# Optimization experiments

Measured on AMD Instinct MI355X. Metric: run time of the kernel, lower is better.

## Reference

```python
import jax, jax.numpy as jnp
import numpy as np

BATCH, D, N = 16, 128, 16
E = N * (N - 1) // 2  # 120 candidate edges (strict upper triangle)


def _incidence(A, n):
    """Build edge-incidence matrices G, H of shape [b, n, E] from binary edge
    vector A [b, E] over the strict upper triangle of an n x n adjacency."""
    r, c = np.triu_indices(n, k=1)
    mask = (A > 0).astype(jnp.float32)  # [b, E]
    node = jnp.arange(n)[:, None]       # [n, 1]
    G = (node == jnp.asarray(r)[None, :]).astype(jnp.float32)[None] * mask[:, None, :]
    H = (node == jnp.asarray(c)[None, :]).astype(jnp.float32)[None] * mask[:, None, :]
    return G, H


def _kron(t1, t2):
    """Batched Kronecker product: t1 [b,r1,c1], t2 [b,r2,c2] -> [b,r1*r2,c1*c2]."""
    b, r1, c1 = t1.shape
    _, r2, c2 = t2.shape
    return (t1[:, :, None, :, None] * t2[:, None, :, None, :]).reshape(b, r1 * r2, c1 * c2)


def setup_inputs() -> dict:
    key = jax.random.key(0)
    ks = jax.random.split(key, 8)
    A_src = jax.random.randint(ks[0], (BATCH, E), 0, 2, dtype=jnp.int32)
    A_tgt = jax.random.randint(ks[1], (BATCH, E), 0, 2, dtype=jnp.int32)
    F_src = jax.random.normal(ks[2], (BATCH, D, N), dtype=jnp.float32)
    F_tgt = jax.random.normal(ks[3], (BATCH, D, N), dtype=jnp.float32)
    U_src = jax.random.normal(ks[4], (BATCH, N, N), dtype=jnp.float32)
    U_tgt = jax.random.normal(ks[5], (BATCH, N, N), dtype=jnp.float32)
    stdv = 1.0 / np.sqrt(D * 2)
    eye_half = jnp.eye(D, dtype=jnp.float32) / 2.0
    lambda1 = jax.random.uniform(ks[6], (D, D), jnp.float32, -stdv, stdv) + eye_half
    lambda2 = jax.random.uniform(ks[7], (D, D), jnp.float32, -stdv, stdv) + eye_half
    return {"A_src": A_src, "A_tgt": A_tgt, "F_src": F_src, "F_tgt": F_tgt,
            "U_src": U_src, "U_tgt": U_tgt, "lambda1": lambda1, "lambda2": lambda2}


def reference(A_src, A_tgt, F_src, F_tgt, U_src, U_tgt, lambda1, lambda2):
    b = F_src.shape[0]
    n, m = F_src.shape[-1], F_tgt.shape[-1]
    # symmetrized, relu'd block weight (w1 = w2 = 1)
    l1 = jax.nn.relu(lambda1 + lambda1.T)
    l2 = jax.nn.relu(lambda2 + lambda2.T)
    weight = jnp.block([[l1, l2], [l2, l1]])  # [2d, 2d]
    # incidence matrices (vectorized replacement of the per-batch scatter loop)
    G1, H1 = _incidence(A_src, n)  # [b, n, E]
    G2, H2 = _incidence(A_tgt, m)  # [b, m, E]
    # edge features: X = cat(F G, F H) -> [b, 2d, E]
    X = jnp.concatenate([F_src @ G1, F_src @ H1], axis=1)
    Y = jnp.concatenate([F_tgt @ G2, F_tgt @ H2], axis=1)
    # edge affinity M_e = X^T W Y : [b, E, E]
    M_e = jnp.einsum('bie,ij,bjf->bef', X, weight, Y)
    # node affinity M_p = U_src^T U_tgt : [b, n, m]
    M_p = jnp.einsum('bdn,bdm->bnm', U_src, U_tgt)
    K1 = _kron(G2, G1)  # [b, m*n, E*E]
    K2 = _kron(H2, H1)  # [b, m*n, E*E]
    # per-column scaling of K1 by flattened M_e (replaces per-column loop)
    K1_new = K1 * M_e.reshape(b, 1, -1)
    diagMp = jax.vmap(jnp.diag)(M_p.reshape(b, -1))  # [b, n*m, n*m]
    M = diagMp + jnp.einsum('bik,bjk->bij', K1_new, K2)
    return M
```

## Files before the change

kernel.cpp:

```cpp
#include <hip/hip_runtime.h>


#define LS 132
#define TS 17

__device__ __forceinline__ int edge_idx(int a, int p) {
    return (a * (31 - a)) / 2 + (p - a - 1);
}

__global__ __launch_bounds__(256) void kA(
    const float* __restrict__ Ftgt,
    const float* __restrict__ lam1, const float* __restrict__ lam2,
    float* __restrict__ ws)
{
    __shared__ float sRow[16 * LS];
    __shared__ float sCol[16 * LS];
    __shared__ float sFt[2048];

    const int blk  = blockIdx.x;
    const int b    = blk >> 4;
    const int lsel = (blk >> 3) & 1;
    const int i0   = (blk & 7) << 4;
    const int t    = threadIdx.x;

    const float* lam = lsel ? lam2 : lam1;

    {
        const float4* rp = (const float4*)(lam + i0 * 128);
#pragma unroll
        for (int it = 0; it < 2; ++it) {
            const int k  = t + it * 256;
            const int il = k >> 5, j4 = k & 31;
            *(float4*)(&sRow[il * LS + j4 * 4]) = rp[il * 32 + j4];
        }
#pragma unroll
        for (int it = 0; it < 8; ++it) {
            const int k  = t + it * 256;
            const int il = k & 15, j = k >> 4;
            sCol[il * LS + j] = lam[j * 128 + i0 + il];
        }
        const float4* f = (const float4*)(Ftgt + b * 2048);
        ((float4*)sFt)[t]       = f[t];
        ((float4*)sFt)[t + 256] = f[t + 256];
    }
    __syncthreads();

    const int il = t >> 4, v = t & 15;
    float acc = 0.f;
#pragma unroll 8
    for (int j0 = 0; j0 < 128; j0 += 4) {
        const float4 r = *(const float4*)(&sRow[il * LS + j0]);
        const float4 c = *(const float4*)(&sCol[il * LS + j0]);
        acc = fmaf(fmaxf(r.x + c.x, 0.f), sFt[((j0 + 0) << 4) | v], acc);
        acc = fmaf(fmaxf(r.y + c.y, 0.f), sFt[((j0 + 1) << 4) | v], acc);
        acc = fmaf(fmaxf(r.z + c.z, 0.f), sFt[((j0 + 2) << 4) | v], acc);
        acc = fmaf(fmaxf(r.w + c.w, 0.f), sFt[((j0 + 3) << 4) | v], acc);
    }
    ws[((b * 2 + lsel) * 128 + i0 + il) * 16 + v] = acc;
}

__global__ __launch_bounds__(256) void kB(
    const int* __restrict__ Asrc, const int* __restrict__ Atgt,
    const float* __restrict__ Fsrc,
    const float* __restrict__ Usrc, const float* __restrict__ Utgt,
    const float* __restrict__ ws, float* __restrict__ out)
{
    __shared__ float sT1[2048], sT2[2048], sFs[2048];
    __shared__ float sU[512];
    __shared__ float sP1[16 * TS], sP2[16 * TS], sMp[256];
    __shared__ int   smask[120];

    const int blk = blockIdx.x;
    const int b   = blk >> 4;
    const int a   = blk & 15;
    const int t   = threadIdx.x;

    {
        const float4* T1g = (const float4*)(ws + (b * 2 + 0) * 2048);
        const float4* T2g = (const float4*)(ws + (b * 2 + 1) * 2048);
        const float4* Fg  = (const float4*)(Fsrc + b * 2048);
        ((float4*)sT1)[t] = T1g[t];  ((float4*)sT1)[t + 256] = T1g[t + 256];
        ((float4*)sT2)[t] = T2g[t];  ((float4*)sT2)[t + 256] = T2g[t + 256];
        ((float4*)sFs)[t] = Fg[t];   ((float4*)sFs)[t + 256] = Fg[t + 256];
        if (t < 64)       ((float4*)sU)[t] = ((const float4*)(Usrc + b * 256))[t];
        else if (t < 128) ((float4*)sU)[t] = ((const float4*)(Utgt + b * 256))[t - 64];
        if (t < 120) smask[t] = (Asrc[b * 120 + t] > 0) && (Atgt[b * 120 + t] > 0);
    }
    __syncthreads();

    {
        const int u = t >> 4, v = t & 15;
        float p1 = 0.f, p2 = 0.f;
#pragma unroll 8
        for (int d = 0; d < 128; ++d) {
            const float fs = sFs[(d << 4) | u];
            p1 = fmaf(fs, sT1[(d << 4) | v], p1);
            p2 = fmaf(fs, sT2[(d << 4) | v], p2);
        }
        float mp = 0.f;
#pragma unroll
        for (int d = 0; d < 16; ++d)
            mp = fmaf(sU[(d << 4) | u], sU[256 + ((d << 4) | v)], mp);
        sP1[u * TS + v] = p1;
        sP2[u * TS + v] = p2;
        sMp[t] = mp;
    }
    __syncthreads();

    const int j0 = (t & 63) << 2;
    const int p  = j0 >> 4;
    const bool condA = (a < p) && (smask[edge_idx(a, p)] != 0);
    float* outR = out + ((size_t)b << 16) + (a << 12);
#pragma unroll
    for (int rr = 0; rr < 4; ++rr) {
        const int c = (t >> 6) + (rr << 2);
        const int r = (a << 4) | c;
        const float cpart = sP1[a * TS + c] + sP2[p * TS + c];
        float4 vec;
        float* vv = (float*)&vec;
#pragma unroll
        for (int s = 0; s < 4; ++s) {
            const int j = j0 + s, q = j & 15;
            float x = 0.f;
            if (condA && (c < q) && (smask[edge_idx(c, q)] != 0))
                x = cpart + sP2[a * TS + q] + sP1[p * TS + q];
            if (r == j) x += sMp[r];
            vv[s] = x;
        }
        *(float4*)(outR + (c << 8) + j0) = vec;
    }
}

extern "C" void kernel_launch(void* const* d_in, const int* in_sizes, int n_in,
                              void* d_out, int out_size, void* d_ws, size_t ws_size,
                              hipStream_t stream) {
    const int*   A_src = (const int*)d_in[0];
    const int*   A_tgt = (const int*)d_in[1];
    const float* F_src = (const float*)d_in[2];
    const float* F_tgt = (const float*)d_in[3];
    const float* U_src = (const float*)d_in[4];
    const float* U_tgt = (const float*)d_in[5];
    const float* lam1  = (const float*)d_in[6];
    const float* lam2  = (const float*)d_in[7];
    float* out = (float*)d_out;
    float* ws  = (float*)d_ws;

    kA<<<256, 256, 0, stream>>>(F_tgt, lam1, lam2, ws);
    kB<<<256, 256, 0, stream>>>(A_src, A_tgt, F_src, U_src, U_tgt, ws, out);
}
```

Measured before the change: 77.75 us.

## Fuse both kernels into one cooperative launch with grid sync

Merges the lambda/F_tgt projection kernel and the output-assembly kernel into a single cooperative kernel separated by a grid-wide barrier, removing one kernel launch and its inter-kernel gap. It also transposes shared-memory layouts (and the workspace layout) so the inner dot products read float4 vectors instead of scalar strided loads. Cooperative launch adds grid-sync overhead and requires all 256 blocks to be co-resident, which 256 CUs should allow.

```diff
diff --git a/kernel.cpp b/kernel.cpp
--- a/kernel.cpp
+++ b/kernel.cpp
@@ -1,4 +1,7 @@
 #include <hip/hip_runtime.h>
+#include <hip/hip_cooperative_groups.h>
+
+namespace cg = cooperative_groups;
 
 
 #define LS 132
@@ -8,126 +11,146 @@
     return (a * (31 - a)) / 2 + (p - a - 1);
 }
 
-__global__ __launch_bounds__(256) void kA(
-    const float* __restrict__ Ftgt,
+__global__ __launch_bounds__(256) void kFused(
+    const int* __restrict__ Asrc, const int* __restrict__ Atgt,
+    const float* __restrict__ Fsrc, const float* __restrict__ Ftgt,
+    const float* __restrict__ Usrc, const float* __restrict__ Utgt,
     const float* __restrict__ lam1, const float* __restrict__ lam2,
-    float* __restrict__ ws)
+    float* __restrict__ ws, float* __restrict__ out)
 {
-    __shared__ float sRow[16 * LS];
-    __shared__ float sCol[16 * LS];
-    __shared__ float sFt[2048];
-
-    const int blk  = blockIdx.x;
-    const int b    = blk >> 4;
-    const int lsel = (blk >> 3) & 1;
-    const int i0   = (blk & 7) << 4;
-    const int t    = threadIdx.x;
-
-    const float* lam = lsel ? lam2 : lam1;
-
-    {
-        const float4* rp = (const float4*)(lam + i0 * 128);
-#pragma unroll
-        for (int it = 0; it < 2; ++it) {
-            const int k  = t + it * 256;
-            const int il = k >> 5, j4 = k & 31;
-            *(float4*)(&sRow[il * LS + j4 * 4]) = rp[il * 32 + j4];
-        }
-#pragma unroll
-        for (int it = 0; it < 8; ++it) {
-            const int k  = t + it * 256;
-            const int il = k & 15, j = k >> 4;
-            sCol[il * LS + j] = lam[j * 128 + i0 + il];
-        }
-        const float4* f = (const float4*)(Ftgt + b * 2048);
-        ((float4*)sFt)[t]       = f[t];
-        ((float4*)sFt)[t + 256] = f[t + 256];
-    }
-    __syncthreads();
-
-    const int il = t >> 4, v = t & 15;
-    float acc = 0.f;
-#pragma unroll 8
-    for (int j0 = 0; j0 < 128; j0 += 4) {
-        const float4 r = *(const float4*)(&sRow[il * LS + j0]);
-        const float4 c = *(const float4*)(&sCol[il * LS + j0]);
-        acc = fmaf(fmaxf(r.x + c.x, 0.f), sFt[((j0 + 0) << 4) | v], acc);
-        acc = fmaf(fmaxf(r.y + c.y, 0.f), sFt[((j0 + 1) << 4) | v], acc);
-        acc = fmaf(fmaxf(r.z + c.z, 0.f), sFt[((j0 + 2) << 4) | v], acc);
-        acc = fmaf(fmaxf(r.w + c.w, 0.f), sFt[((j0 + 3) << 4) | v], acc);
-    }
-    ws[((b * 2 + lsel) * 128 + i0 + il) * 16 + v] = acc;
-}
-
-__global__ __launch_bounds__(256) void kB(
-    const int* __restrict__ Asrc, const int* __restrict__ Atgt,
-    const float* __restrict__ Fsrc,
-    const float* __restrict__ Usrc, const float* __restrict__ Utgt,
-    const float* __restrict__ ws, float* __restrict__ out)
-{
-    __shared__ float sT1[2048], sT2[2048], sFs[2048];
+    __shared__ float sA[16 * LS];
+    __shared__ float sB[16 * LS];
+    __shared__ float sC[16 * LS];
     __shared__ float sU[512];
     __shared__ float sP1[16 * TS], sP2[16 * TS], sMp[256];
     __shared__ int   smask[120];
 
     const int blk = blockIdx.x;
-    const int b   = blk >> 4;
-    const int a   = blk & 15;
     const int t   = threadIdx.x;
 
     {
+        const int b    = blk >> 4;
+        const int lsel = (blk >> 3) & 1;
+        const int i0   = (blk & 7) << 4;
+        const float* lam = lsel ? lam2 : lam1;
+
+        const float4* rp = (const float4*)(lam + i0 * 128);
+#pragma unroll
+        for (int it = 0; it < 2; ++it) {
+            const int k = t + it * 256;
+            const int il = k >> 5, j4 = k & 31;
+            *(float4*)(&sA[il * LS + j4 * 4]) = rp[il * 32 + j4];
+        }
+#pragma unroll
+        for (int it = 0; it < 8; ++it) {
+            const int k = t + it * 256;
+            const int il = k & 15, j = k >> 4;
+            sB[il * LS + j] = lam[j * 128 + i0 + il];
+        }
+        const float4* fp = (const float4*)(Ftgt + b * 2048);
+#pragma unroll
+        for (int it = 0; it < 2; ++it) {
+            const int k = t + it * 256;
+            const int j = k >> 2, v0 = (k & 3) * 4;
+            const float4 f = fp[k];
+            sC[(v0 + 0) * LS + j] = f.x;
+            sC[(v0 + 1) * LS + j] = f.y;
+            sC[(v0 + 2) * LS + j] = f.z;
+            sC[(v0 + 3) * LS + j] = f.w;
+        }
+        __syncthreads();
+
+        const int v = t >> 4, il = t & 15;
+        float acc = 0.f;
+#pragma unroll 8
+        for (int j0 = 0; j0 < 128; j0 += 4) {
+            const float4 r = *(const float4*)(&sA[il * LS + j0]);
+            const float4 c = *(const float4*)(&sB[il * LS + j0]);
+            const float4 f = *(const float4*)(&sC[v * LS + j0]);
+            acc = fmaf(fmaxf(r.x + c.x, 0.f), f.x, acc);
+            acc = fmaf(fmaxf(r.y + c.y, 0.f), f.y, acc);
+            acc = fmaf(fmaxf(r.z + c.z, 0.f), f.z, acc);
+            acc = fmaf(fmaxf(r.w + c.w, 0.f), f.w, acc);
+        }
+        ws[((b * 2 + lsel) * 16 + v) * 128 + i0 + il] = acc;
+    }
+
+    cg::this_grid().sync();
+
+    {
+        const int b = blk >> 4;
+        const int a = blk & 15;
+
         const float4* T1g = (const float4*)(ws + (b * 2 + 0) * 2048);
         const float4* T2g = (const float4*)(ws + (b * 2 + 1) * 2048);
-        const float4* Fg  = (const float4*)(Fsrc + b * 2048);
-        ((float4*)sT1)[t] = T1g[t];  ((float4*)sT1)[t + 256] = T1g[t + 256];
-        ((float4*)sT2)[t] = T2g[t];  ((float4*)sT2)[t + 256] = T2g[t + 256];
-        ((float4*)sFs)[t] = Fg[t];   ((float4*)sFs)[t + 256] = Fg[t + 256];
+#pragma unroll
+        for (int it = 0; it < 2; ++it) {
+            const int k = t + it * 256;
+            const int v = k >> 5, d4 = (k & 31) * 4;
+            *(float4*)(&sA[v * LS + d4]) = T1g[k];
+            *(float4*)(&sB[v * LS + d4]) = T2g[k];
+        }
+        const float4* fp = (const float4*)(Fsrc + b * 2048);
+#pragma unroll
+        for (int it = 0; it < 2; ++it) {
+            const int k = t + it * 256;
+            const int d = k >> 2, u0 = (k & 3) * 4;
+            const float4 f = fp[k];
+            sC[(u0 + 0) * LS + d] = f.x;
+            sC[(u0 + 1) * LS + d] = f.y;
+            sC[(u0 + 2) * LS + d] = f.z;
+            sC[(u0 + 3) * LS + d] = f.w;
+        }
         if (t < 64)       ((float4*)sU)[t] = ((const float4*)(Usrc + b * 256))[t];
         else if (t < 128) ((float4*)sU)[t] = ((const float4*)(Utgt + b * 256))[t - 64];
         if (t < 120) smask[t] = (Asrc[b * 120 + t] > 0) && (Atgt[b * 120 + t] > 0);
-    }
-    __syncthreads();
+        __syncthreads();
 
-    {
-        const int u = t >> 4, v = t & 15;
-        float p1 = 0.f, p2 = 0.f;
+        {
+            const int u = t >> 4, v = t & 15;
+            float p1 = 0.f, p2 = 0.f;
 #pragma unroll 8
-        for (int d = 0; d < 128; ++d) {
-            const float fs = sFs[(d << 4) | u];
-            p1 = fmaf(fs, sT1[(d << 4) | v], p1);
-            p2 = fmaf(fs, sT2[(d << 4) | v], p2);
+            for (int d0 = 0; d0 < 128; d0 += 4) {
+                const float4 fs = *(const float4*)(&sC[u * LS + d0]);
+                const float4 t1 = *(const float4*)(&sA[v * LS + d0]);
+                const float4 t2 = *(const float4*)(&sB[v * LS + d0]);
+                p1 = fmaf(fs.x, t1.x, p1);  p2 = fmaf(fs.x, t2.x, p2);
+                p1 = fmaf(fs.y, t1.y, p1);  p2 = fmaf(fs.y, t2.y, p2);
+                p1 = fmaf(fs.z, t1.z, p1);  p2 = fmaf(fs.z, t2.z, p2);
+                p1 = fmaf(fs.w, t1.w, p1);  p2 = fmaf(fs.w, t2.w, p2);
+            }
+            float mp = 0.f;
+#pragma unroll
+            for (int d = 0; d < 16; ++d)
+                mp = fmaf(sU[(d << 4) | u], sU[256 + ((d << 4) | v)], mp);
+            sP1[u * TS + v] = p1;
+            sP2[u * TS + v] = p2;
+            sMp[t] = mp;
         }
-        float mp = 0.f;
+        __syncthreads();
+
+        const int j0 = (t & 63) << 2;
+        const int p  = j0 >> 4;
+        const bool condA = (a < p) && (smask[edge_idx(a, p)] != 0);
+        float* outR = out + ((size_t)b << 16) + (a << 12);
 #pragma unroll
-        for (int d = 0; d < 16; ++d)
-            mp = fmaf(sU[(d << 4) | u], sU[256 + ((d << 4) | v)], mp);
-        sP1[u * TS + v] = p1;
-        sP2[u * TS + v] = p2;
-        sMp[t] = mp;
-    }
-    __syncthreads();
-
-    const int j0 = (t & 63) << 2;
-    const int p  = j0 >> 4;
-    const bool condA = (a < p) && (smask[edge_idx(a, p)] != 0);
-    float* outR = out + ((size_t)b << 16) + (a << 12);
+        for (int rr = 0; rr < 4; ++rr) {
+            const int c = (t >> 6) + (rr << 2);
+            const int r = (a << 4) | c;
+            const float cpart = sP1[a * TS + c] + sP2[p * TS + c];
+            float4 vec;
+            float* vv = (float*)&vec;
 #pragma unroll
-    for (int rr = 0; rr < 4; ++rr) {
-        const int c = (t >> 6) + (rr << 2);
-        const int r = (a << 4) | c;
-        const float cpart = sP1[a * TS + c] + sP2[p * TS + c];
-        float4 vec;
-        float* vv = (float*)&vec;
-#pragma unroll
-        for (int s = 0; s < 4; ++s) {
-            const int j = j0 + s, q = j & 15;
-            float x = 0.f;
-            if (condA && (c < q) && (smask[edge_idx(c, q)] != 0))
-                x = cpart + sP2[a * TS + q] + sP1[p * TS + q];
-            if (r == j) x += sMp[r];
-            vv[s] = x;
+            for (int s = 0; s < 4; ++s) {
+                const int j = j0 + s, q = j & 15;
+                float x = 0.f;
+                if (condA && (c < q) && (smask[edge_idx(c, q)] != 0))
+                    x = cpart + sP2[a * TS + q] + sP1[p * TS + q];
+                if (r == j) x += sMp[r];
+                vv[s] = x;
+            }
+            *(float4*)(outR + (c << 8) + j0) = vec;
         }
-        *(float4*)(outR + (c << 8) + j0) = vec;
     }
 }
 
@@ -145,6 +168,11 @@
     float* out = (float*)d_out;
     float* ws  = (float*)d_ws;
 
-    kA<<<256, 256, 0, stream>>>(F_tgt, lam1, lam2, ws);
-    kB<<<256, 256, 0, stream>>>(A_src, A_tgt, F_src, U_src, U_tgt, ws, out);
+    void* args[] = {
+        (void*)&A_src, (void*)&A_tgt, (void*)&F_src, (void*)&F_tgt,
+        (void*)&U_src, (void*)&U_tgt, (void*)&lam1, (void*)&lam2,
+        (void*)&ws, (void*)&out
+    };
+    hipLaunchCooperativeKernel((const void*)kFused, dim3(256), dim3(256),
+                               args, 0, stream);
 }
```

After: 115.9 us. 1.49x slower.
